# Kernel tuning notes

Measured on AMD Instinct MI355X. Metric: run time of the kernel, lower is better.

## Reference

```python
import jax, jax.numpy as jnp
import numpy as np

STRIDE = (4, 4)
MASK = (17, 17)
G_MEAN = 85.384
G_STD = 53.798
LEV = 5  # len(bins)
EPS = 1e-8
_BINS = np.array([0.0, 0.5, G_MEAN - G_STD, G_MEAN, G_MEAN + G_STD], dtype=np.float32)
_DISTS = [1, 2, 4]
_THETAS = [0.0, np.pi / 4, np.pi / 2, 3 * np.pi / 4]
# skimage greycomatrix offsets: (row, col) = (round(sin(t)*d), round(cos(t)*d)), dist-major
OFFSETS = [(int(round(np.sin(t) * d)), int(round(np.cos(t) * d))) for d in _DISTS for t in _THETAS]


def setup_inputs():
    key = jax.random.key(0)
    x = jax.random.uniform(key, (8, 1, 512, 512), dtype=jnp.float32) * 255.0
    return {"inputs": x}


def _sliding_windows(x):
    B, C, H, W = x.shape
    nx = (H - MASK[0]) // STRIDE[0] + 1
    ny = (W - MASK[1]) // STRIDE[1] + 1
    rows = (jnp.arange(nx) * STRIDE[0])[:, None] + jnp.arange(MASK[0])  # (nx, Mx)
    cols = (jnp.arange(ny) * STRIDE[1])[:, None] + jnp.arange(MASK[1])  # (ny, My)
    w = x[:, :, rows]              # (B, C, nx, Mx, W)
    w = w[:, :, :, :, cols]        # (B, C, nx, Mx, ny, My)
    return jnp.transpose(w, (0, 1, 2, 4, 3, 5))  # (B, C, nx, ny, Mx, My)


def _statistics(w):
    m = w.mean(axis=(-2, -1))
    s = w.std(axis=(-2, -1))
    mx = w.max(axis=(-2, -1))
    mn = w.min(axis=(-2, -1))
    # Faithful to original: mean is rescaled in-place BEFORE being used in max/min stats
    m = m / G_MEAN
    s = s / G_STD
    mx = (mx - m) / G_STD
    mn = (m - mn) / G_STD
    return jnp.concatenate([m, s, mx, mn], axis=1)  # (B, 4*C, nx, ny)


def _glcm(qf, dr, dc):
    # qf: (Wn, Mx, My) int32 -> normalized symmetric GLCM (Wn, LEV, LEV)
    Mx, My = qf.shape[-2:]
    if dc >= 0:
        a = qf[:, :Mx - dr, :My - dc]
        b = qf[:, dr:, dc:]
    else:
        a = qf[:, :Mx - dr, -dc:]
        b = qf[:, dr:, :My + dc]
    Wn = qf.shape[0]
    code = (a * LEV + b).reshape(Wn, -1)
    flat = (jnp.arange(Wn, dtype=jnp.int32)[:, None] * (LEV * LEV) + code).reshape(-1)
    cnt = jax.ops.segment_sum(jnp.ones(flat.shape, jnp.float32), flat, num_segments=Wn * LEV * LEV)
    G = cnt.reshape(Wn, LEV, LEV)
    G = G + jnp.swapaxes(G, -1, -2)  # symmetric=True
    return G / jnp.sum(G, axis=(-2, -1), keepdims=True)  # normed=True


def _hist_glcm_features(q):
    # q: (B, C, nx, ny, Mx, My) int32 -> (B, 64, nx, ny) (C must be 1)
    B, C, nx, ny, Mx, My = q.shape
    qf = q.reshape(-1, Mx, My)
    Wn = qf.shape[0]
    G = jnp.stack([_glcm(qf, dr, dc) for dr, dc in OFFSETS], axis=1)  # (Wn, 12, L, L)

    I = jnp.arange(LEV, dtype=jnp.float32)
    d2 = (I[:, None] - I[None, :]) ** 2
    contrast = jnp.einsum('wkij,ij->wk', G, d2)
    homogeneity = jnp.einsum('wkij,ij->wk', G, 1.0 / (1.0 + d2))
    energy = jnp.sqrt(jnp.sum(G * G, axis=(-2, -1)))
    Pi = G.sum(axis=-1)   # (Wn, 12, L)
    Pj = G.sum(axis=-2)
    mu_i = jnp.sum(I * Pi, axis=-1)
    mu_j = jnp.sum(I * Pj, axis=-1)
    di = I[None, None, :] - mu_i[..., None]
    dj = I[None, None, :] - mu_j[..., None]
    std_i = jnp.sqrt(jnp.sum(Pi * di * di, axis=-1))
    std_j = jnp.sqrt(jnp.sum(Pj * dj * dj, axis=-1))
    cov = jnp.einsum('wkij,wki,wkj->wk', G, di, dj)
    denom = std_i * std_j
    correlation = jnp.where(denom < 1e-15, 1.0, cov / jnp.maximum(denom, 1e-30))
    entropy = -jnp.sum(G * jnp.log2(G + EPS), axis=(-2, -1))  # (Wn, 12)

    qv = qf.reshape(Wn, -1)
    cnts = jnp.stack([jnp.sum(qv == k, axis=-1) for k in range(1, LEV)], axis=-1).astype(jnp.float32)
    tot = cnts.sum(axis=-1, keepdims=True)
    hist = jnp.where(tot > 0, cnts / jnp.maximum(tot, 1.0), 0.0)  # (Wn, LEV-1)

    feat = jnp.concatenate([hist, contrast, homogeneity, energy, correlation, entropy], axis=-1)
    feat = feat.reshape(B, C, nx, ny, -1)
    return jnp.transpose(feat, (0, 4, 2, 3, 1))[..., 0]  # (B, 64, nx, ny)


def reference(inputs):
    w = _sliding_windows(inputs)                                   # (B,C,nx,ny,17,17)
    stat = _statistics(w)                                          # (B,4,nx,ny)
    q = (jnp.digitize(w, jnp.asarray(_BINS)) - 1).astype(jnp.int32)
    hg = _hist_glcm_features(q)                                    # (B,64,nx,ny)
    feats = jnp.concatenate([stat, hg], axis=1)                    # (B,68,nx,ny)
    return jnp.mean(feats, axis=(-2, -1))                          # (B,68)
```

## Files before the change

kernel.cpp:

```cpp
#include <hip/hip_runtime.h>


#define G_MEAN_F 85.384f
#define G_STD_F  53.798f
#define MASK_WS_BYTES (8u * 512u * 36u * 8u)

__device__ constexpr int LO15[15] = {0,0,0,0,0,1,1,1,1,2,2,2,3,3,4};
__device__ constexpr int HI15[15] = {0,1,2,3,4,1,2,3,4,2,3,4,3,4,4};

__device__ __forceinline__ float wred(float v) {
#pragma unroll
  for (int m = 32; m; m >>= 1) v += __shfl_xor(v, m, 64);
  return v;
}

__device__ __forceinline__ void load_row(const unsigned long long* mrow, int ly4, unsigned m[5]) {
  unsigned long long a = mrow[0], b = mrow[1], c = mrow[2], d = mrow[3];
  m[1] = (unsigned)(a >> ly4) & 0x1FFFFu;
  m[2] = (unsigned)(b >> ly4) & 0x1FFFFu;
  m[3] = (unsigned)(c >> ly4) & 0x1FFFFu;
  m[4] = (unsigned)(d >> ly4) & 0x1FFFFu;
  m[0] = 0x1FFFFu & ~(m[1] | m[2] | m[3] | m[4]);
}

__device__ __forceinline__ void upd(unsigned cnt[15], const unsigned a[5], const unsigned b[5]) {
#pragma unroll
  for (int u = 0; u < 15; ++u) {
    const int i = LO15[u], j = HI15[u];
    unsigned s = __popc(a[i] & b[j]);
    if (i != j) s += __popc(a[j] & b[i]);
    cnt[u] += s;
  }
}

template<int DC>
__device__ __forceinline__ void updoff(unsigned cnt[15], const unsigned a[5], const unsigned b[5]) {
  unsigned as[5], bs[5];
#pragma unroll
  for (int v = 0; v < 5; ++v) {
    as[v] = (DC < 0) ? (a[v] >> (-DC)) : a[v];
    bs[v] = (DC > 0) ? (b[v] >> DC) : b[v];
  }
  upd(cnt, as, bs);
}

__device__ __forceinline__ void emit(const unsigned cnt[15], float Np, bool valid,
                                     float* pt0, int k0, int k1) {
  const float invN = 1.0f / Np;
  const float inv2N = 0.5f / Np;
  float con = 0.0f, hom = 0.0f, eac = 0.0f, ent = 0.0f;
  float P[5] = {0, 0, 0, 0, 0};
#pragma unroll
  for (int u = 0; u < 15; ++u) {
    const int lo = LO15[u], hi = HI15[u];
    const float m = (float)cnt[u];
    const float d2 = (float)((hi - lo) * (hi - lo));
    con += m * d2;
    hom += m * (1.0f / (1.0f + d2));
    if (lo == hi) {
      eac += m * m;
      P[lo] += 2.0f * m;
      float g = m * invN;
      ent -= g * __log2f(g + 1e-8f);
    } else {
      eac += 0.5f * m * m;
      P[lo] += m; P[hi] += m;
      float g = m * inv2N;
      ent -= 2.0f * g * __log2f(g + 1e-8f);
    }
  }
  con *= invN;
  hom *= invN;
  float ene = sqrtf(eac) * invN;
  float mu = 0.0f;
#pragma unroll
  for (int i = 0; i < 5; ++i) { P[i] *= inv2N; mu += (float)i * P[i]; }
  float s2 = 0.0f;
#pragma unroll
  for (int i = 0; i < 5; ++i) { float d = (float)i - mu; s2 = fmaf(P[i] * d, d, s2); }
  float sd = sqrtf(s2);
  float denom = sd * sd;
  float cov = 0.0f;
#pragma unroll
  for (int u = 0; u < 15; ++u)
    cov += ((float)cnt[u] * invN) * ((float)LO15[u] - mu) * ((float)HI15[u] - mu);
  float corr = (denom < 1e-15f) ? 1.0f : cov / fmaxf(denom, 1e-30f);

  if (!valid) { con = 0; hom = 0; ene = 0; corr = 0; ent = 0; }
  con = wred(con); hom = wred(hom); ene = wred(ene); corr = wred(corr); ent = wred(ent);
  if ((threadIdx.x & 63) == 0) {
    const float s = 1.0f / 15376.0f;
    pt0[(8 + k0) * 256] = con * s;
    pt0[(20 + k0) * 256] = hom * s;
    pt0[(32 + k0) * 256] = ene * s;
    pt0[(44 + k0) * 256] = corr * s;
    pt0[(56 + k0) * 256] = ent * s;
    if (k1 >= 0) {
      pt0[(8 + k1) * 256] = con * s;
      pt0[(20 + k1) * 256] = hom * s;
      pt0[(32 + k1) * 256] = ene * s;
      pt0[(44 + k1) * 256] = corr * s;
      pt0[(56 + k1) * 256] = ent * s;
    }
  }
}

template<int DRA, int DCA, int DRB, int DCB>
__device__ __forceinline__ void glcm_dual1(const unsigned long long* mbase, int ly4,
                                           float NpA, float NpB, bool valid, float* pt0,
                                           int kA0, int kA1, int kB0, int kB1) {
  unsigned cntA[15], cntB[15];
#pragma unroll
  for (int u = 0; u < 15; ++u) { cntA[u] = 0; cntB[u] = 0; }
  unsigned p[5], c[5];
  load_row(mbase, ly4, p);
  if (DRA == 0) updoff<DCA>(cntA, p, p);
  if (DRB == 0) updoff<DCB>(cntB, p, p);
#pragma unroll 1
  for (int r = 1; r < 17; ++r) {
    load_row(mbase + r * 5, ly4, c);
    updoff<DCA>(cntA, DRA ? p : c, c);
    updoff<DCB>(cntB, DRB ? p : c, c);
#pragma unroll
    for (int v = 0; v < 5; ++v) p[v] = c[v];
  }
  emit(cntA, NpA, valid, pt0, kA0, kA1);
  emit(cntB, NpB, valid, pt0, kB0, kB1);
}

template<int DR, int DC>
__device__ __forceinline__ void glcm_one(const unsigned long long* mbase, int ly4,
                                         float Np, bool valid, float* pt0, int k0, int k1) {
  unsigned cnt[15];
#pragma unroll
  for (int u = 0; u < 15; ++u) cnt[u] = 0;
  unsigned buf[DR + 1][5];
#pragma unroll
  for (int r = 0; r < DR; ++r) load_row(mbase + r * 5, ly4, buf[r]);
#pragma unroll 1
  for (int r = DR; r < 17; ++r) {
    load_row(mbase + r * 5, ly4, buf[DR]);
    updoff<DC>(cnt, buf[0], buf[DR]);
#pragma unroll
    for (int i = 0; i < DR; ++i)
#pragma unroll
      for (int v = 0; v < 5; ++v) buf[i][v] = buf[i + 1][v];
  }
  emit(cnt, Np, valid, pt0, k0, k1);
}

__global__ __launch_bounds__(64)
void mask_build_kernel(const float* __restrict__ x, unsigned long long* __restrict__ mg) {
  const int lane = threadIdx.x;
  const int r = blockIdx.x;
  const int b = blockIdx.y;
  const float* xr = x + ((size_t)b * 512 + r) * 512;
  unsigned long long* mr = mg + ((size_t)b * 512 + r) * 36;

  const float T1 = 0.5f;
  const float T2 = (float)(85.384 - 53.798);
  const float T3 = 85.384f;
  const float T4 = (float)(85.384 + 53.798);

#pragma unroll 1
  for (int seg = 0; seg < 8; ++seg) {
    float xv = xr[seg * 64 + lane];
    int q = (int)(xv >= T1) + (int)(xv >= T2) + (int)(xv >= T3) + (int)(xv >= T4);
    unsigned long long b1 = __ballot(q == 1);
    unsigned long long b2 = __ballot(q == 2);
    unsigned long long b3 = __ballot(q == 3);
    unsigned long long b4 = __ballot(q == 4);
    if (lane < 4) {
      unsigned long long bv = (lane == 0) ? b1 : (lane == 1) ? b2 : (lane == 2) ? b3 : b4;
      mr[seg * 4 + lane] = bv;
    }
  }
  if (lane < 4) mr[32 + lane] = 0;
}

__global__ __launch_bounds__(128)
void glcm_feat_kernel(const float* __restrict__ x,
                      const unsigned long long* __restrict__ mg,
                      float* __restrict__ part) {
  __shared__ unsigned long long masks[45 * 5];

  const int tid = threadIdx.x;
  const int lane = tid & 63;
  const int wid = tid >> 6;
  const int role = blockIdx.x >> 4;
  const int tyx = blockIdx.x & 15;
  const int b = blockIdx.z;
  const int px0 = blockIdx.y * 32;
  const int py0 = tyx * 32;
  const float* xb = x + (size_t)b * 512 * 512;

  const int s0 = py0 >> 6;
  const int sh = py0 & 63;
  const unsigned long long* mgb = mg + (size_t)b * 512 * 36;
#pragma unroll 1
  for (int t = tid; t < 180; t += 128) {
    int row = t >> 2, lev = t & 3;
    int gr = px0 + row; if (gr > 511) gr = 511;
    const unsigned long long* p = mgb + (size_t)gr * 36 + s0 * 4 + lev;
    unsigned long long w0 = p[0];
    unsigned long long w1 = p[4];
    masks[row * 5 + lev] = sh ? ((w0 >> 32) | (w1 << 32)) : w0;
  }
  __syncthreads();

  const int lx = lane >> 3, ly = lane & 7;
  const int wx = blockIdx.y * 8 + lx;
  const int wy = tyx * 8 + ly;
  const bool valid = (wx < 124) && (wy < 124);
  const unsigned long long* mbase = masks + (lx * 4) * 5;
  const int ly4 = ly * 4;
  const int tile = blockIdx.y * 16 + tyx;
  float* pt0 = part + (size_t)b * 68 * 256 + tile;

  if (role == 0) {
    if (wid == 0) {
      unsigned nv1 = 0, nv2 = 0, nv3 = 0, nv4 = 0;
#pragma unroll 1
      for (int r = 0; r < 17; ++r) {
        unsigned m[5];
        load_row(mbase + r * 5, ly4, m);
        nv1 += __popc(m[1]); nv2 += __popc(m[2]);
        nv3 += __popc(m[3]); nv4 += __popc(m[4]);
      }
      unsigned tot = nv1 + nv2 + nv3 + nv4;
      float ti = (tot > 0) ? 1.0f / (float)tot : 0.0f;
      float h1 = (float)nv1 * ti, h2 = (float)nv2 * ti;
      float h3 = (float)nv3 * ti, h4 = (float)nv4 * ti;

      int r0 = px0 + lx * 4; if (r0 > 495) r0 = 495;
      int c0 = py0 + ly * 4; if (c0 > 492) c0 = 492;
      const float* fw = xb + (size_t)r0 * 512 + c0;
      float sum = 0.0f, ssq = 0.0f, mx = -1e30f, mn = 1e30f;
#pragma unroll 1
      for (int r = 0; r < 17; ++r) {
        const float* p = fw + r * 512;
        const float4* p4 = (const float4*)p;
#pragma unroll
        for (int w = 0; w < 4; ++w) {
          float4 f = p4[w];
          sum += f.x; ssq = fmaf(f.x, f.x, ssq); mx = fmaxf(mx, f.x); mn = fminf(mn, f.x);
          sum += f.y; ssq = fmaf(f.y, f.y, ssq); mx = fmaxf(mx, f.y); mn = fminf(mn, f.y);
          sum += f.z; ssq = fmaf(f.z, f.z, ssq); mx = fmaxf(mx, f.z); mn = fminf(mn, f.z);
          sum += f.w; ssq = fmaf(f.w, f.w, ssq); mx = fmaxf(mx, f.w); mn = fminf(mn, f.w);
        }
        float t = p[16];
        sum += t; ssq = fmaf(t, t, ssq); mx = fmaxf(mx, t); mn = fminf(mn, t);
      }
      float mean = sum * (1.0f / 289.0f);
      float var = fmaxf(ssq * (1.0f / 289.0f) - mean * mean, 0.0f);
      float fm = mean / G_MEAN_F;
      float fs = sqrtf(var) / G_STD_F;
      float fmx = (mx - fm) / G_STD_F;
      float fmn = (fm - mn) / G_STD_F;
      if (!valid) { fm = fs = fmx = fmn = h1 = h2 = h3 = h4 = 0.0f; }
      fm = wred(fm); fs = wred(fs); fmx = wred(fmx); fmn = wred(fmn);
      h1 = wred(h1); h2 = wred(h2); h3 = wred(h3); h4 = wred(h4);
      if (lane == 0) {
        const float s = 1.0f / 15376.0f;
        pt0[0 * 256] = fm * s;
        pt0[1 * 256] = fs * s;
        pt0[2 * 256] = fmx * s;
        pt0[3 * 256] = fmn * s;
        pt0[4 * 256] = h1 * s;
        pt0[5 * 256] = h2 * s;
        pt0[6 * 256] = h3 * s;
        pt0[7 * 256] = h4 * s;
      }
    } else {
      glcm_dual1<0, 1, 1, 0>(mbase, ly4, 272.0f, 272.0f, valid, pt0, 0, -1, 2, -1);
    }
  } else if (role == 1) {
    if (wid == 0) {
      glcm_dual1<0, 2, 1, 1>(mbase, ly4, 255.0f, 256.0f, valid, pt0, 4, -1, 1, 5);
    } else {
      glcm_dual1<0, 4, 1, -1>(mbase, ly4, 221.0f, 256.0f, valid, pt0, 8, -1, 3, 7);
    }
  } else {
    if (wid == 0) {
      glcm_one<2, 0>(mbase, ly4, 255.0f, valid, pt0, 6, -1);
      glcm_one<3, 3>(mbase, ly4, 196.0f, valid, pt0, 9, -1);
    } else {
      glcm_one<4, 0>(mbase, ly4, 221.0f, valid, pt0, 10, -1);
      glcm_one<3, -3>(mbase, ly4, 196.0f, valid, pt0, 11, -1);
    }
  }
}

__global__ __launch_bounds__(64)
void reduce_kernel(const float* __restrict__ part, float* __restrict__ out) {
  const int ch = blockIdx.x;
  const int b = blockIdx.y;
  const int lane = threadIdx.x;
  const float4* p = (const float4*)(part + ((size_t)b * 68 + ch) * 256);
  float4 f = p[lane];
  float v = (f.x + f.y) + (f.z + f.w);
  v = wred(v);
  if (lane == 0) out[b * 68 + ch] = v;
}

extern "C" void kernel_launch(void* const* d_in, const int* in_sizes, int n_in,
                              void* d_out, int out_size, void* d_ws, size_t ws_size,
                              hipStream_t stream)
{
  const float* x = (const float*)d_in[0];
  float* out = (float*)d_out;
  unsigned long long* mg = (unsigned long long*)d_ws;
  float* part = (float*)((char*)d_ws + MASK_WS_BYTES);

  mask_build_kernel<<<dim3(512, 8), dim3(64), 0, stream>>>(x, mg);
  glcm_feat_kernel<<<dim3(48, 16, 8), dim3(128), 0, stream>>>(x, mg, part);
  reduce_kernel<<<dim3(68, 8), dim3(64), 0, stream>>>(part, out);
}
```

Before: 119.8 us.

## Share overlapping window rows between vertically adjacent window pairs per thread

Each thread now handles two vertically adjacent windows (offset by 4 rows) and accumulates the GLCM counts and statistics in three segments: head, shared middle and tail. The shared middle rows are counted once and added to both windows, which cuts per-window popcount work and global float reads roughly in half for the overlap. The grid is halved in x, shared memory grows to 77 rows, and the per-tile partials shrink to 128. Smaller tweaks also OR disjoint masks before a single popc and drop a redundant sqrt in the correlation. The trade-offs are fewer blocks, which may hurt occupancy, and more live registers from the three count arrays.

```diff
diff --git a/kernel.cpp b/kernel.cpp
--- a/kernel.cpp
+++ b/kernel.cpp
@@ -27,28 +27,35 @@
 #pragma unroll
   for (int u = 0; u < 15; ++u) {
     const int i = LO15[u], j = HI15[u];
-    unsigned s = __popc(a[i] & b[j]);
-    if (i != j) s += __popc(a[j] & b[i]);
-    cnt[u] += s;
-  }
-}
-
-template<int DC>
-__device__ __forceinline__ void updoff(unsigned cnt[15], const unsigned a[5], const unsigned b[5]) {
+    unsigned t = a[i] & b[j];
+    if (i != j) t |= a[j] & b[i];
+    cnt[u] += __popc(t);
+  }
+}
+
+template<int DR, int DC>
+__device__ __forceinline__ void row_pair(unsigned cnt[15], const unsigned long long* mk,
+                                         int row, int ly4) {
+  unsigned a[5], b[5];
+  load_row(mk + row * 5, ly4, a);
+  if (DR > 0) load_row(mk + (row + DR) * 5, ly4, b);
   unsigned as[5], bs[5];
 #pragma unroll
   for (int v = 0; v < 5; ++v) {
+    unsigned bb = (DR > 0) ? b[v] : a[v];
     as[v] = (DC < 0) ? (a[v] >> (-DC)) : a[v];
-    bs[v] = (DC > 0) ? (b[v] >> DC) : b[v];
+    bs[v] = (DC > 0) ? (bb >> DC) : bb;
   }
   upd(cnt, as, bs);
 }
 
-__device__ __forceinline__ void emit(const unsigned cnt[15], float Np, bool valid,
-                                     float* pt0, int k0, int k1) {
+__device__ __forceinline__ void feat5(const unsigned cnt[15], float Np,
+                                      float& con, float& hom, float& ene,
+                                      float& corr, float& ent) {
   const float invN = 1.0f / Np;
   const float inv2N = 0.5f / Np;
-  float con = 0.0f, hom = 0.0f, eac = 0.0f, ent = 0.0f;
+  con = 0.0f; hom = 0.0f; ent = 0.0f;
+  float eac = 0.0f;
   float P[5] = {0, 0, 0, 0, 0};
 #pragma unroll
   for (int u = 0; u < 15; ++u) {
@@ -71,82 +78,63 @@
   }
   con *= invN;
   hom *= invN;
-  float ene = sqrtf(eac) * invN;
+  ene = sqrtf(eac) * invN;
   float mu = 0.0f;
 #pragma unroll
   for (int i = 0; i < 5; ++i) { P[i] *= inv2N; mu += (float)i * P[i]; }
   float s2 = 0.0f;
 #pragma unroll
   for (int i = 0; i < 5; ++i) { float d = (float)i - mu; s2 = fmaf(P[i] * d, d, s2); }
-  float sd = sqrtf(s2);
-  float denom = sd * sd;
+  float denom = s2;
   float cov = 0.0f;
 #pragma unroll
   for (int u = 0; u < 15; ++u)
     cov += ((float)cnt[u] * invN) * ((float)LO15[u] - mu) * ((float)HI15[u] - mu);
-  float corr = (denom < 1e-15f) ? 1.0f : cov / fmaxf(denom, 1e-30f);
-
-  if (!valid) { con = 0; hom = 0; ene = 0; corr = 0; ent = 0; }
-  con = wred(con); hom = wred(hom); ene = wred(ene); corr = wred(corr); ent = wred(ent);
+  corr = (denom < 1e-15f) ? 1.0f : cov / fmaxf(denom, 1e-30f);
+}
+
+__device__ __forceinline__ void emit2(const unsigned c1[15], const unsigned c2[15], float Np,
+                                      bool v1, bool v2, float* pt0, int k0, int k1) {
+  float con1, hom1, ene1, cor1, ent1, con2, hom2, ene2, cor2, ent2;
+  feat5(c1, Np, con1, hom1, ene1, cor1, ent1);
+  feat5(c2, Np, con2, hom2, ene2, cor2, ent2);
+  if (!v1) { con1 = 0; hom1 = 0; ene1 = 0; cor1 = 0; ent1 = 0; }
+  if (!v2) { con2 = 0; hom2 = 0; ene2 = 0; cor2 = 0; ent2 = 0; }
+  float con = wred(con1 + con2), hom = wred(hom1 + hom2), ene = wred(ene1 + ene2);
+  float cor = wred(cor1 + cor2), ent = wred(ent1 + ent2);
   if ((threadIdx.x & 63) == 0) {
     const float s = 1.0f / 15376.0f;
-    pt0[(8 + k0) * 256] = con * s;
-    pt0[(20 + k0) * 256] = hom * s;
-    pt0[(32 + k0) * 256] = ene * s;
-    pt0[(44 + k0) * 256] = corr * s;
-    pt0[(56 + k0) * 256] = ent * s;
+    pt0[(8 + k0) * 128] = con * s;
+    pt0[(20 + k0) * 128] = hom * s;
+    pt0[(32 + k0) * 128] = ene * s;
+    pt0[(44 + k0) * 128] = cor * s;
+    pt0[(56 + k0) * 128] = ent * s;
     if (k1 >= 0) {
-      pt0[(8 + k1) * 256] = con * s;
-      pt0[(20 + k1) * 256] = hom * s;
-      pt0[(32 + k1) * 256] = ene * s;
-      pt0[(44 + k1) * 256] = corr * s;
-      pt0[(56 + k1) * 256] = ent * s;
-    }
-  }
-}
-
-template<int DRA, int DCA, int DRB, int DCB>
-__device__ __forceinline__ void glcm_dual1(const unsigned long long* mbase, int ly4,
-                                           float NpA, float NpB, bool valid, float* pt0,
-                                           int kA0, int kA1, int kB0, int kB1) {
-  unsigned cntA[15], cntB[15];
-#pragma unroll
-  for (int u = 0; u < 15; ++u) { cntA[u] = 0; cntB[u] = 0; }
-  unsigned p[5], c[5];
-  load_row(mbase, ly4, p);
-  if (DRA == 0) updoff<DCA>(cntA, p, p);
-  if (DRB == 0) updoff<DCB>(cntB, p, p);
-#pragma unroll 1
-  for (int r = 1; r < 17; ++r) {
-    load_row(mbase + r * 5, ly4, c);
-    updoff<DCA>(cntA, DRA ? p : c, c);
-    updoff<DCB>(cntB, DRB ? p : c, c);
-#pragma unroll
-    for (int v = 0; v < 5; ++v) p[v] = c[v];
-  }
-  emit(cntA, NpA, valid, pt0, kA0, kA1);
-  emit(cntB, NpB, valid, pt0, kB0, kB1);
+      pt0[(8 + k1) * 128] = con * s;
+      pt0[(20 + k1) * 128] = hom * s;
+      pt0[(32 + k1) * 128] = ene * s;
+      pt0[(44 + k1) * 128] = cor * s;
+      pt0[(56 + k1) * 128] = ent * s;
+    }
+  }
 }
 
 template<int DR, int DC>
-__device__ __forceinline__ void glcm_one(const unsigned long long* mbase, int ly4,
-                                         float Np, bool valid, float* pt0, int k0, int k1) {
-  unsigned cnt[15];
-#pragma unroll
-  for (int u = 0; u < 15; ++u) cnt[u] = 0;
-  unsigned buf[DR + 1][5];
-#pragma unroll
-  for (int r = 0; r < DR; ++r) load_row(mbase + r * 5, ly4, buf[r]);
-#pragma unroll 1
-  for (int r = DR; r < 17; ++r) {
-    load_row(mbase + r * 5, ly4, buf[DR]);
-    updoff<DC>(cnt, buf[0], buf[DR]);
-#pragma unroll
-    for (int i = 0; i < DR; ++i)
-#pragma unroll
-      for (int v = 0; v < 5; ++v) buf[i][v] = buf[i + 1][v];
-  }
-  emit(cnt, Np, valid, pt0, k0, k1);
+__device__ __forceinline__ void glcm_pass(const unsigned long long* mk, int s, int ly4,
+                                          float Np, bool v1, bool v2, float* pt0,
+                                          int k0, int k1) {
+  unsigned A[15], S[15], B[15];
+#pragma unroll
+  for (int u = 0; u < 15; ++u) { A[u] = 0; S[u] = 0; B[u] = 0; }
+#pragma unroll 1
+  for (int R = 0; R < 4; ++R) row_pair<DR, DC>(A, mk, s + R, ly4);
+#pragma unroll 1
+  for (int R = 4; R < 17 - DR; ++R) row_pair<DR, DC>(S, mk, s + R, ly4);
+#pragma unroll 1
+  for (int R = 17 - DR; R < 21 - DR; ++R) row_pair<DR, DC>(B, mk, s + R, ly4);
+#pragma unroll
+  for (int u = 0; u < 15; ++u) { A[u] += S[u]; B[u] += S[u]; }
+  emit2(A, B, Np, v1, v2, pt0, k0, k1);
 }
 
 __global__ __launch_bounds__(64)
@@ -182,23 +170,24 @@
 void glcm_feat_kernel(const float* __restrict__ x,
                       const unsigned long long* __restrict__ mg,
                       float* __restrict__ part) {
-  __shared__ unsigned long long masks[45 * 5];
+  __shared__ unsigned long long masks[77 * 5];
 
   const int tid = threadIdx.x;
   const int lane = tid & 63;
   const int wid = tid >> 6;
   const int role = blockIdx.x >> 4;
-  const int tyx = blockIdx.x & 15;
+  const int ty = blockIdx.x & 15;
+  const int tx = blockIdx.y;
   const int b = blockIdx.z;
-  const int px0 = blockIdx.y * 32;
-  const int py0 = tyx * 32;
+  const int px0 = tx * 64;
+  const int py0 = ty * 32;
   const float* xb = x + (size_t)b * 512 * 512;
 
   const int s0 = py0 >> 6;
   const int sh = py0 & 63;
   const unsigned long long* mgb = mg + (size_t)b * 512 * 36;
 #pragma unroll 1
-  for (int t = tid; t < 180; t += 128) {
+  for (int t = tid; t < 77 * 4; t += 128) {
     int row = t >> 2, lev = t & 3;
     int gr = px0 + row; if (gr > 511) gr = 511;
     const unsigned long long* p = mgb + (size_t)gr * 36 + s0 * 4 + lev;
@@ -208,85 +197,102 @@
   }
   __syncthreads();
 
-  const int lx = lane >> 3, ly = lane & 7;
-  const int wx = blockIdx.y * 8 + lx;
-  const int wy = tyx * 8 + ly;
-  const bool valid = (wx < 124) && (wy < 124);
-  const unsigned long long* mbase = masks + (lx * 4) * 5;
+  const int lxp = lane >> 3, ly = lane & 7;
+  const int wx1 = tx * 16 + 2 * lxp;
+  const int wy = ty * 8 + ly;
+  const bool vy = (wy < 124);
+  const bool v1 = (wx1 < 124) && vy;
+  const bool v2 = (wx1 + 1 < 124) && vy;
+  const int s = 8 * lxp;
   const int ly4 = ly * 4;
-  const int tile = blockIdx.y * 16 + tyx;
-  float* pt0 = part + (size_t)b * 68 * 256 + tile;
+  const int tile = tx * 16 + ty;
+  float* pt0 = part + (size_t)b * 68 * 128 + tile;
 
   if (role == 0) {
     if (wid == 0) {
-      unsigned nv1 = 0, nv2 = 0, nv3 = 0, nv4 = 0;
-#pragma unroll 1
-      for (int r = 0; r < 17; ++r) {
+      unsigned hA[4] = {0,0,0,0}, hS[4] = {0,0,0,0}, hB[4] = {0,0,0,0};
+#pragma unroll 1
+      for (int R = 0; R < 21; ++R) {
         unsigned m[5];
-        load_row(mbase + r * 5, ly4, m);
-        nv1 += __popc(m[1]); nv2 += __popc(m[2]);
-        nv3 += __popc(m[3]); nv4 += __popc(m[4]);
+        load_row(masks + (s + R) * 5, ly4, m);
+        unsigned* h = (R < 4) ? hA : (R < 17) ? hS : hB;
+#pragma unroll
+        for (int v = 0; v < 4; ++v) h[v] += __popc(m[v + 1]);
       }
-      unsigned tot = nv1 + nv2 + nv3 + nv4;
-      float ti = (tot > 0) ? 1.0f / (float)tot : 0.0f;
-      float h1 = (float)nv1 * ti, h2 = (float)nv2 * ti;
-      float h3 = (float)nv3 * ti, h4 = (float)nv4 * ti;
-
-      int r0 = px0 + lx * 4; if (r0 > 495) r0 = 495;
-      int c0 = py0 + ly * 4; if (c0 > 492) c0 = 492;
-      const float* fw = xb + (size_t)r0 * 512 + c0;
-      float sum = 0.0f, ssq = 0.0f, mx = -1e30f, mn = 1e30f;
-#pragma unroll 1
-      for (int r = 0; r < 17; ++r) {
+      int sp = px0 + s; if (sp > 488) sp = 488;
+      int c0 = py0 + ly4; if (c0 > 492) c0 = 492;
+      const float* fw = xb + (size_t)sp * 512 + c0;
+      float sA = 0, qA = 0, sS = 0, qS = 0, sB = 0, qB = 0;
+      float mxA = -1e30f, mnA = 1e30f, mxS = -1e30f, mnS = 1e30f, mxB = -1e30f, mnB = 1e30f;
+#pragma unroll 1
+      for (int r = 0; r < 21; ++r) {
         const float* p = fw + r * 512;
         const float4* p4 = (const float4*)p;
+        float rs = 0, rq = 0, rmx = -1e30f, rmn = 1e30f;
 #pragma unroll
         for (int w = 0; w < 4; ++w) {
           float4 f = p4[w];
-          sum += f.x; ssq = fmaf(f.x, f.x, ssq); mx = fmaxf(mx, f.x); mn = fminf(mn, f.x);
-          sum += f.y; ssq = fmaf(f.y, f.y, ssq); mx = fmaxf(mx, f.y); mn = fminf(mn, f.y);
-          sum += f.z; ssq = fmaf(f.z, f.z, ssq); mx = fmaxf(mx, f.z); mn = fminf(mn, f.z);
-          sum += f.w; ssq = fmaf(f.w, f.w, ssq); mx = fmaxf(mx, f.w); mn = fminf(mn, f.w);
+          rs += f.x; rq = fmaf(f.x, f.x, rq); rmx = fmaxf(rmx, f.x); rmn = fminf(rmn, f.x);
+          rs += f.y; rq = fmaf(f.y, f.y, rq); rmx = fmaxf(rmx, f.y); rmn = fminf(rmn, f.y);
+          rs += f.z; rq = fmaf(f.z, f.z, rq); rmx = fmaxf(rmx, f.z); rmn = fminf(rmn, f.z);
+          rs += f.w; rq = fmaf(f.w, f.w, rq); rmx = fmaxf(rmx, f.w); rmn = fminf(rmn, f.w);
         }
         float t = p[16];
-        sum += t; ssq = fmaf(t, t, ssq); mx = fmaxf(mx, t); mn = fminf(mn, t);
+        rs += t; rq = fmaf(t, t, rq); rmx = fmaxf(rmx, t); rmn = fminf(rmn, t);
+        if (r < 4)       { sA += rs; qA += rq; mxA = fmaxf(mxA, rmx); mnA = fminf(mnA, rmn); }
+        else if (r < 17) { sS += rs; qS += rq; mxS = fmaxf(mxS, rmx); mnS = fminf(mnS, rmn); }
+        else             { sB += rs; qB += rq; mxB = fmaxf(mxB, rmx); mnB = fminf(mnB, rmn); }
       }
-      float mean = sum * (1.0f / 289.0f);
-      float var = fmaxf(ssq * (1.0f / 289.0f) - mean * mean, 0.0f);
-      float fm = mean / G_MEAN_F;
-      float fs = sqrtf(var) / G_STD_F;
-      float fmx = (mx - fm) / G_STD_F;
-      float fmn = (fm - mn) / G_STD_F;
-      if (!valid) { fm = fs = fmx = fmn = h1 = h2 = h3 = h4 = 0.0f; }
-      fm = wred(fm); fs = wred(fs); fmx = wred(fmx); fmn = wred(fmn);
-      h1 = wred(h1); h2 = wred(h2); h3 = wred(h3); h4 = wred(h4);
-      if (lane == 0) {
-        const float s = 1.0f / 15376.0f;
-        pt0[0 * 256] = fm * s;
-        pt0[1 * 256] = fs * s;
-        pt0[2 * 256] = fmx * s;
-        pt0[3 * 256] = fmn * s;
-        pt0[4 * 256] = h1 * s;
-        pt0[5 * 256] = h2 * s;
-        pt0[6 * 256] = h3 * s;
-        pt0[7 * 256] = h4 * s;
+      float ch[8][2];
+#pragma unroll
+      for (int w = 0; w < 2; ++w) {
+        float sum = w ? (sS + sB) : (sA + sS);
+        float ssq = w ? (qS + qB) : (qA + qS);
+        float mx = w ? fmaxf(mxS, mxB) : fmaxf(mxA, mxS);
+        float mn = w ? fminf(mnS, mnB) : fminf(mnA, mnS);
+        unsigned t1 = w ? (hS[0] + hB[0]) : (hA[0] + hS[0]);
+        unsigned t2 = w ? (hS[1] + hB[1]) : (hA[1] + hS[1]);
+        unsigned t3 = w ? (hS[2] + hB[2]) : (hA[2] + hS[2]);
+        unsigned t4 = w ? (hS[3] + hB[3]) : (hA[3] + hS[3]);
+        float mean = sum * (1.0f / 289.0f);
+        float var = fmaxf(ssq * (1.0f / 289.0f) - mean * mean, 0.0f);
+        float fm = mean / G_MEAN_F;
+        ch[0][w] = fm;
+        ch[1][w] = sqrtf(var) / G_STD_F;
+        ch[2][w] = (mx - fm) / G_STD_F;
+        ch[3][w] = (fm - mn) / G_STD_F;
+        unsigned tot = t1 + t2 + t3 + t4;
+        float ti = (tot > 0) ? 1.0f / (float)tot : 0.0f;
+        ch[4][w] = (float)t1 * ti;
+        ch[5][w] = (float)t2 * ti;
+        ch[6][w] = (float)t3 * ti;
+        ch[7][w] = (float)t4 * ti;
+      }
+#pragma unroll
+      for (int c = 0; c < 8; ++c) {
+        float f = (v1 ? ch[c][0] : 0.0f) + (v2 ? ch[c][1] : 0.0f);
+        f = wred(f);
+        if (lane == 0) pt0[c * 128] = f * (1.0f / 15376.0f);
       }
     } else {
-      glcm_dual1<0, 1, 1, 0>(mbase, ly4, 272.0f, 272.0f, valid, pt0, 0, -1, 2, -1);
+      glcm_pass<0, 1>(masks, s, ly4, 272.0f, v1, v2, pt0, 0, -1);
+      glcm_pass<1, 0>(masks, s, ly4, 272.0f, v1, v2, pt0, 2, -1);
     }
   } else if (role == 1) {
     if (wid == 0) {
-      glcm_dual1<0, 2, 1, 1>(mbase, ly4, 255.0f, 256.0f, valid, pt0, 4, -1, 1, 5);
+      glcm_pass<0, 2>(masks, s, ly4, 255.0f, v1, v2, pt0, 4, -1);
+      glcm_pass<1, 1>(masks, s, ly4, 256.0f, v1, v2, pt0, 1, 5);
     } else {
-      glcm_dual1<0, 4, 1, -1>(mbase, ly4, 221.0f, 256.0f, valid, pt0, 8, -1, 3, 7);
+      glcm_pass<0, 4>(masks, s, ly4, 221.0f, v1, v2, pt0, 8, -1);
+      glcm_pass<1, -1>(masks, s, ly4, 256.0f, v1, v2, pt0, 3, 7);
     }
   } else {
     if (wid == 0) {
-      glcm_one<2, 0>(mbase, ly4, 255.0f, valid, pt0, 6, -1);
-      glcm_one<3, 3>(mbase, ly4, 196.0f, valid, pt0, 9, -1);
+      glcm_pass<2, 0>(masks, s, ly4, 255.0f, v1, v2, pt0, 6, -1);
+      glcm_pass<3, 3>(masks, s, ly4, 196.0f, v1, v2, pt0, 9, -1);
     } else {
-      glcm_one<4, 0>(mbase, ly4, 221.0f, valid, pt0, 10, -1);
-      glcm_one<3, -3>(mbase, ly4, 196.0f, valid, pt0, 11, -1);
+      glcm_pass<4, 0>(masks, s, ly4, 221.0f, v1, v2, pt0, 10, -1);
+      glcm_pass<3, -3>(masks, s, ly4, 196.0f, v1, v2, pt0, 11, -1);
     }
   }
 }
@@ -296,9 +302,9 @@
   const int ch = blockIdx.x;
   const int b = blockIdx.y;
   const int lane = threadIdx.x;
-  const float4* p = (const float4*)(part + ((size_t)b * 68 + ch) * 256);
-  float4 f = p[lane];
-  float v = (f.x + f.y) + (f.z + f.w);
+  const float2* p = (const float2*)(part + ((size_t)b * 68 + ch) * 128);
+  float2 f = p[lane];
+  float v = f.x + f.y;
   v = wred(v);
   if (lane == 0) out[b * 68 + ch] = v;
 }
@@ -313,6 +319,6 @@
   float* part = (float*)((char*)d_ws + MASK_WS_BYTES);
 
   mask_build_kernel<<<dim3(512, 8), dim3(64), 0, stream>>>(x, mg);
-  glcm_feat_kernel<<<dim3(48, 16, 8), dim3(128), 0, stream>>>(x, mg, part);
+  glcm_feat_kernel<<<dim3(48, 8, 8), dim3(128), 0, stream>>>(x, mg, part);
   reduce_kernel<<<dim3(68, 8), dim3(64), 0, stream>>>(part, out);
 }
```

After: 114.3 us. -4.6%, faster.
